# Optimization experiments

Hardware: AMD Instinct MI355X
Metric: run time of the kernel (lower is better)

Reference implementation:

```python
import jax, jax.numpy as jnp
import numpy as np

B, LQ, LK = 16, 1024, 2048
E, F, A = 512, 256, 512


def setup_inputs() -> dict:
    key = jax.random.key(0)
    ks = jax.random.split(key, 8)
    s_e = 1.0 / np.sqrt(E)
    s_f = 1.0 / np.sqrt(F)
    s_a = 1.0 / np.sqrt(A)
    return {
        "lstm_embeddings": jax.random.normal(ks[0], (B, LQ, E), jnp.float32),
        "optical_flow_features": jax.random.normal(ks[1], (B, LK, F), jnp.float32),
        "Wq": jax.random.normal(ks[2], (E, A), jnp.float32) * s_e,
        "bq": jnp.zeros((A,), jnp.float32),
        "Wk": jax.random.normal(ks[3], (F, A), jnp.float32) * s_f,
        "bk": jnp.zeros((A,), jnp.float32),
        "Wv": jax.random.normal(ks[4], (F, A), jnp.float32) * s_f,
        "bv": jnp.zeros((A,), jnp.float32),
        "Wo": jax.random.normal(ks[5], (A, E), jnp.float32) * s_a,
        "bo": jnp.zeros((E,), jnp.float32),
    }


def reference(lstm_embeddings, optical_flow_features, Wq, bq, Wk, bk, Wv, bv, Wo, bo):
    # Linear projections (x @ W + b), matching nn.Linear with W stored as [in, out]
    q = lstm_embeddings @ Wq + bq            # [B, LQ, A]
    k = optical_flow_features @ Wk + bk      # [B, LK, A]
    v = optical_flow_features @ Wv + bv      # [B, LK, A]
    # NOTE: original module does NOT scale scores by 1/sqrt(A) — stay faithful.
    scores = jnp.einsum("bqa,bka->bqk", q, k)      # [B, LQ, LK]
    weights = jax.nn.softmax(scores, axis=-1)
    context = jnp.einsum("bqk,bka->bqa", weights, v)  # [B, LQ, A]
    return context @ Wo + bo                          # [B, LQ, E]
```

## Files before the change

### kernel.cpp

```cpp
#include <hip/hip_runtime.h>


#define DEV static __device__ __forceinline__

typedef __attribute__((ext_vector_type(8))) short s8v;
typedef __attribute__((ext_vector_type(8))) _Float16 h8v;
typedef __attribute__((ext_vector_type(4))) float f4v;
typedef __attribute__((ext_vector_type(16))) float f16f;
typedef __attribute__((ext_vector_type(4))) float float4v;
typedef __attribute__((ext_vector_type(4))) unsigned int u32x4;
typedef unsigned short u16;
typedef unsigned int u32;

constexpr int BB = 16;
constexpr int LQ = 1024;
constexpr int LK = 2048;
constexpr int E = 512;
constexpr int F = 256;

DEV u16 f2bf(float x) {
    u32 u = __builtin_bit_cast(u32, x);
    u += 0x7fff + ((u >> 16) & 1);
    return (u16)(u >> 16);
}
DEV float bf2f(u16 h) { return __builtin_bit_cast(float, (u32)h << 16); }

DEV f4v MF(s8v a, s8v b, f4v c) {
    return __builtin_amdgcn_mfma_f32_16x16x32_bf16(a, b, c, 0, 0, 0);
}
DEV f4v MF16(h8v a, h8v b, f4v c) {
    return __builtin_amdgcn_mfma_f32_16x16x32_f16(a, b, c, 0, 0, 0);
}
DEV f16f MF32(h8v a, h8v b, f16f c) {
    return __builtin_amdgcn_mfma_f32_32x32x16_f16(a, b, c, 0, 0, 0);
}
DEV u32 pkh(float a, float b) {
    auto t = __builtin_amdgcn_cvt_pkrtz(a, b);
    return __builtin_bit_cast(u32, t);
}

DEV void gll16(const _Float16* g, _Float16* l) {
    __builtin_amdgcn_global_load_lds(
        (const __attribute__((address_space(1))) u32*)g,
        (__attribute__((address_space(3))) u32*)l, 16, 0, 0);
}

__global__ __launch_bounds__(256) void prew(
    const float* __restrict__ y, _Float16* __restrict__ yA,
    _Float16* __restrict__ yB,
    const float* __restrict__ Wq, const float* __restrict__ bq,
    const float* __restrict__ Wk, const float* __restrict__ Wv,
    const float* __restrict__ bv, const float* __restrict__ Wo,
    const float* __restrict__ bo,
    u16* __restrict__ Mhb, u16* __restrict__ Ntb,
    float* __restrict__ wvec, float* __restrict__ cvec)
{
    __shared__ __align__(16) char smem[33536];
    const int tid = threadIdx.x;
    const int bi = blockIdx.x;

    if (bi < 1024) {
        float (*Y)[260] = (float(*)[260])smem;
        const int b = bi >> 6, t = bi & 63;
        const float* src = y + ((size_t)b * LK + t * 32) * F;
#pragma unroll
        for (int i = 0; i < 8; ++i) {
            int base = i * 1024 + tid * 4;
            int k = base >> 8, f = base & 255;
            *(float4v*)&Y[k][f] = *(const float4v*)(src + base);
        }
        __syncthreads();
        size_t tb = (size_t)(b * 64 + t) * 8192;
#pragma unroll
        for (int i = 0; i < 4; ++i) {
            int c = i * 256 + tid;
            int k = c & 31, hi = (c >> 5) & 1, fs = c >> 6;
            int f0 = fs * 16 + hi * 8;
            float4v v0 = *(const float4v*)&Y[k][f0];
            float4v v1 = *(const float4v*)&Y[k][f0 + 4];
            h8v v;
#pragma unroll
            for (int j = 0; j < 4; ++j) { v[j] = (_Float16)v0[j]; v[4 + j] = (_Float16)v1[j]; }
            *(h8v*)(yA + tb + (size_t)c * 8) = v;
        }
#pragma unroll
        for (int i = 0; i < 4; ++i) {
            int c = i * 256 + tid;
            int fl = c & 31, hi = (c >> 5) & 1, frag = c >> 6;
            int ft = frag >> 1, ks = frag & 1;
            int f = ft * 32 + fl, k0 = ks * 16 + hi * 8;
            h8v v;
#pragma unroll
            for (int j = 0; j < 8; ++j) v[j] = (_Float16)Y[k0 + j][f];
            *(h8v*)(yB + tb + (size_t)c * 8) = v;
        }
        return;
    }

    const int wb = bi - 1024;
    if (wb >= 64) {
        if (wb == 64) {
            const float* r = Wk + (size_t)tid * 512;
            float s = 0.f;
#pragma unroll 4
            for (int a = 0; a < 512; a += 4) {
                float4v v = *(const float4v*)(r + a);
                float4v bb = *(const float4v*)(bq + a);
                s += v[0] * bb[0] + v[1] * bb[1] + v[2] * bb[2] + v[3] * bb[3];
            }
            wvec[tid] = s;
        } else {
            int e = (wb - 65) * 256 + tid;
            float s = bo[e];
#pragma unroll 4
            for (int a = 0; a < 512; ++a) s += bv[a] * Wo[(size_t)a * 512 + e];
            cvec[e] = s;
        }
        return;
    }

    const bool ntm = wb >= 32;
    const int bj = ntm ? wb - 32 : wb;
    const int m0 = ntm ? (bj >> 2) * 64 : (bj >> 3) * 64;
    const int n0 = ntm ? (bj & 3) * 64 : (bj & 7) * 64;
    const float* Ag = ntm ? Wo : Wk;
    const float* Bg = ntm ? Wv : Wq;

    u16 (*Ash)[40] = (u16(*)[40])(smem);
    u16 (*Asl)[40] = (u16(*)[40])(smem + 5120);
    u16 (*Bsh)[40] = (u16(*)[40])(smem + 10240);
    u16 (*Bsl)[40] = (u16(*)[40])(smem + 15360);

    const int w = tid >> 6, lane = tid & 63;
    const int g = lane >> 4, qn = lane & 15;
    const int wr = w & 1, wc = w >> 1;

    f4v acc[2][2];
#pragma unroll
    for (int i = 0; i < 2; ++i)
#pragma unroll
        for (int j = 0; j < 2; ++j) acc[i][j] = (f4v){0.f, 0.f, 0.f, 0.f};

    for (int k0 = 0; k0 < 512; k0 += 32) {
        __syncthreads();
        if (!ntm) {
            int r = tid & 63, c = (tid >> 6) * 8;
            const float* s = Ag + (size_t)(m0 + r) * 512 + k0 + c;
            float4v v0 = *(const float4v*)s, v1 = *(const float4v*)(s + 4);
            short hh[8], ll[8];
#pragma unroll
            for (int i = 0; i < 8; ++i) {
                float x = (i < 4) ? v0[i] : v1[i - 4];
                u16 h = f2bf(x);
                hh[i] = (short)h;
                ll[i] = (short)f2bf(x - bf2f(h));
            }
            *(s8v*)&Ash[r][c] = (s8v){hh[0],hh[1],hh[2],hh[3],hh[4],hh[5],hh[6],hh[7]};
            *(s8v*)&Asl[r][c] = (s8v){ll[0],ll[1],ll[2],ll[3],ll[4],ll[5],ll[6],ll[7]};
        } else {
            int k = tid >> 3, mc = (tid & 7) * 8;
            const float* s = Ag + (size_t)(k0 + k) * 512 + m0 + mc;
            float4v v0 = *(const float4v*)s, v1 = *(const float4v*)(s + 4);
#pragma unroll
            for (int i = 0; i < 8; ++i) {
                float x = (i < 4) ? v0[i] : v1[i - 4];
                u16 h = f2bf(x);
                Ash[mc + i][k] = h;
                Asl[mc + i][k] = f2bf(x - bf2f(h));
            }
        }
        {
            int r = tid & 63, c = (tid >> 6) * 8;
            const float* s = Bg + (size_t)(n0 + r) * 512 + k0 + c;
            float4v v0 = *(const float4v*)s, v1 = *(const float4v*)(s + 4);
            short hh[8], ll[8];
#pragma unroll
            for (int i = 0; i < 8; ++i) {
                float x = (i < 4) ? v0[i] : v1[i - 4];
                u16 h = f2bf(x);
                hh[i] = (short)h;
                ll[i] = (short)f2bf(x - bf2f(h));
            }
            *(s8v*)&Bsh[r][c] = (s8v){hh[0],hh[1],hh[2],hh[3],hh[4],hh[5],hh[6],hh[7]};
            *(s8v*)&Bsl[r][c] = (s8v){ll[0],ll[1],ll[2],ll[3],ll[4],ll[5],ll[6],ll[7]};
        }
        __syncthreads();

        s8v ah[2], al[2], bh[2], bl[2];
#pragma unroll
        for (int mt = 0; mt < 2; ++mt) {
            ah[mt] = *(const s8v*)&Ash[wr * 32 + mt * 16 + qn][g * 8];
            al[mt] = *(const s8v*)&Asl[wr * 32 + mt * 16 + qn][g * 8];
        }
#pragma unroll
        for (int nt = 0; nt < 2; ++nt) {
            bh[nt] = *(const s8v*)&Bsh[wc * 32 + nt * 16 + qn][g * 8];
            bl[nt] = *(const s8v*)&Bsl[wc * 32 + nt * 16 + qn][g * 8];
        }
#pragma unroll
        for (int mt = 0; mt < 2; ++mt)
#pragma unroll
            for (int nt = 0; nt < 2; ++nt) {
                acc[mt][nt] = MF(ah[mt], bh[nt], acc[mt][nt]);
                acc[mt][nt] = MF(ah[mt], bl[nt], acc[mt][nt]);
                acc[mt][nt] = MF(al[mt], bh[nt], acc[mt][nt]);
            }
    }

#pragma unroll
    for (int mt = 0; mt < 2; ++mt)
#pragma unroll
        for (int nt = 0; nt < 2; ++nt)
#pragma unroll
            for (int r = 0; r < 4; ++r) {
                int gm = m0 + wr * 32 + mt * 16 + 4 * g + r;
                int gn = n0 + wc * 32 + nt * 16 + qn;
                float v = acc[mt][nt][r];
                if (!ntm) {
                    size_t off = (size_t)((gn >> 5) * 16 + (gm >> 4)) * 512 +
                                 (gm & 15) * 8 + ((gn >> 3) & 3) * 128 + (gn & 7);
                    Mhb[off] = __builtin_bit_cast(u16, (_Float16)v);
                } else {
                    size_t off = (size_t)((gn >> 5) * 32 + (gm >> 4)) * 512 +
                                 (gm & 15) * 8 + ((gn >> 3) & 3) * 128 + (gn & 7);
                    Ntb[off] = __builtin_bit_cast(u16, (_Float16)v);
                }
            }
}

__global__ __launch_bounds__(256) void qprime5(
    const float* __restrict__ x, const u16* __restrict__ Mhb,
    const float* __restrict__ wv, _Float16* __restrict__ q16)
{
    __shared__ _Float16 Xs[2][64][40];
    const int tid = threadIdx.x, w = tid >> 6, lane = tid & 63;
    const int g = lane >> 4, qn = lane & 15;
    const int m0 = blockIdx.x * 64;
    const int nh = blockIdx.y * 8;
    const int srow = tid >> 2, scol = (tid & 3) * 8;
    const _Float16* Mh = (const _Float16*)Mhb;

    f4v acc[8];
#pragma unroll
    for (int n = 0; n < 8; ++n) acc[n] = (f4v){0.f, 0.f, 0.f, 0.f};

    float4v a0, a1;
    auto LDA = [&](int k0) {
        const float* s = x + (size_t)(m0 + srow) * 512 + k0 + scol;
        a0 = *(const float4v*)s;
        a1 = *(const float4v*)(s + 4);
    };
    auto STA = [&](int buf) {
        h8v v;
#pragma unroll
        for (int j = 0; j < 4; ++j) { v[j] = (_Float16)a0[j]; v[4 + j] = (_Float16)a1[j]; }
        *(h8v*)&Xs[buf][srow][scol] = v;
    };

    LDA(0); STA(0); LDA(32);
    __syncthreads();

    for (int t = 0; t < 16; ++t) {
        const int cur = t & 1;
        h8v af = *(const h8v*)&Xs[cur][w * 16 + qn][g * 8];
        const int fb = t * 16 + nh;
#pragma unroll
        for (int nt = 0; nt < 8; ++nt) {
            h8v bf = *(const h8v*)(Mh + (size_t)(fb + nt) * 512 + lane * 8);
            acc[nt] = MF16(af, bf, acc[nt]);
        }
        if (t < 15) {
            STA(cur ^ 1);
            if (t < 14) LDA((t + 2) * 32);
            __syncthreads();
        }
    }

#pragma unroll
    for (int nt = 0; nt < 8; ++nt) {
        int col = (nh + nt) * 16 + qn;
        float wvc = wv[col];
#pragma unroll
        for (int r = 0; r < 4; ++r) {
            int row = m0 + w * 16 + 4 * g + r;
            q16[(size_t)row * 256 + col] =
                (_Float16)((acc[nt][r] + wvc) * 1.44269504f);
        }
    }
}

__global__ __launch_bounds__(512) void flash6(
    const _Float16* __restrict__ q16, const _Float16* __restrict__ yA,
    const _Float16* __restrict__ yB, _Float16* __restrict__ part,
    float* __restrict__ ml)
{
    __shared__ _Float16 Asb[2][2][8192];
    __shared__ _Float16 Bsb[2][2][8192];

    const int tid = threadIdx.x;
    const int lane = tid & 63;
    const int q32 = lane & 31;
    const int hi = lane >> 5;

    int id = blockIdx.x;
    int xcd = id & 7, slot = id >> 3;
    int grp = xcd + 8 * (slot >> 2);
    int qb = slot & 3;
    int b = grp >> 2, z = grp & 3;
    const int qw = qb * 256 + (tid >> 6) * 32;

    h8v qf[16];
    {
        const _Float16* qp = q16 + ((size_t)b * LQ + qw + q32) * 256 + hi * 8;
#pragma unroll
        for (int s = 0; s < 16; ++s) qf[s] = *(const h8v*)(qp + s * 16);
    }
    f16f ctx[8];
#pragma unroll
    for (int i = 0; i < 8; ++i) ctx[i] = (f16f){};
    float mrun = -3.0e38f, lrun = 0.f;

    const size_t tbe = (size_t)(b * 64 + z * 16) * 8192;

    auto STAGE = [&](int sup, int buf) {
#pragma unroll
        for (int j = 0; j < 2; ++j) {
            const _Float16* ga = yA + tbe + (size_t)(sup * 2 + j) * 8192 + tid * 8;
            const _Float16* gb = yB + tbe + (size_t)(sup * 2 + j) * 8192 + tid * 8;
            gll16(ga,        &Asb[buf][j][tid * 8]);
            gll16(ga + 4096, &Asb[buf][j][tid * 8 + 4096]);
            gll16(gb,        &Bsb[buf][j][tid * 8]);
            gll16(gb + 4096, &Bsb[buf][j][tid * 8 + 4096]);
        }
    };

    STAGE(0, 0);
    __syncthreads();

    int buf = 0;
    for (int s = 0; s < 8; ++s) {
        if (s < 7) STAGE(s + 1, buf ^ 1);
#pragma unroll
        for (int j = 0; j < 2; ++j) {
            const _Float16* Ap = &Asb[buf][j][0];
            const _Float16* Bp = &Bsb[buf][j][0];
            f16f Sa = (f16f){}, Sb = (f16f){};
#pragma unroll
            for (int fs = 0; fs < 16; fs += 2) {
                h8v a0 = *(const h8v*)(Ap + fs * 512 + lane * 8);
                h8v a1 = *(const h8v*)(Ap + (fs + 1) * 512 + lane * 8);
                Sa = MF32(a0, qf[fs], Sa);
                Sb = MF32(a1, qf[fs + 1], Sb);
            }
            f16f S = Sa + Sb;
            float mt = fmaxf(S[0], S[1]);
#pragma unroll
            for (int r = 2; r < 16; ++r) mt = fmaxf(mt, S[r]);
            mt = fmaxf(mt, __shfl_xor(mt, 32));
            if (!__all(mt <= mrun + 11.5416f)) {
                float mnew = fmaxf(mrun, mt);
                float alpha = exp2f(mrun - mnew);
                lrun *= alpha;
#pragma unroll
                for (int r = 0; r < 16; ++r) {
                    int qr = (r & 3) + 8 * (r >> 2) + 4 * hi;
                    float ar = __shfl(alpha, qr);
#pragma unroll
                    for (int ft = 0; ft < 8; ++ft) ctx[ft][r] *= ar;
                }
                mrun = mnew;
            }
            float p[16], ps = 0.f;
#pragma unroll
            for (int r = 0; r < 16; ++r) { p[r] = exp2f(S[r] - mrun); ps += p[r]; }
            ps += __shfl_xor(ps, 32);
            lrun += ps;
            {
                u32 X0 = pkh(p[0], p[1]),   X1 = pkh(p[2], p[3]);
                u32 Y0 = pkh(p[4], p[5]),   Y1 = pkh(p[6], p[7]);
                u32 Z0 = pkh(p[8], p[9]),   Z1 = pkh(p[10], p[11]);
                u32 W0 = pkh(p[12], p[13]), W1 = pkh(p[14], p[15]);
                u32 M0 = hi ? X0 : Y0, M1 = hi ? X1 : Y1;
                u32 N0 = hi ? Z0 : W0, N1 = hi ? Z1 : W1;
                u32 sM0 = __shfl_xor(M0, 32), sM1 = __shfl_xor(M1, 32);
                u32 sN0 = __shfl_xor(N0, 32), sN1 = __shfl_xor(N1, 32);
                u32x4 A0u = (u32x4){hi ? sM0 : X0, hi ? sM1 : X1,
                                    hi ? Y0 : sM0, hi ? Y1 : sM1};
                u32x4 A1u = (u32x4){hi ? sN0 : Z0, hi ? sN1 : Z1,
                                    hi ? W0 : sN0, hi ? W1 : sN1};
                h8v pa0 = __builtin_bit_cast(h8v, A0u);
                h8v pa1 = __builtin_bit_cast(h8v, A1u);
#pragma unroll
                for (int ft = 0; ft < 8; ++ft) {
                    h8v bf = *(const h8v*)(Bp + (ft * 2 + 0) * 512 + lane * 8);
                    ctx[ft] = MF32(pa0, bf, ctx[ft]);
                }
#pragma unroll
                for (int ft = 0; ft < 8; ++ft) {
                    h8v bf = *(const h8v*)(Bp + (ft * 2 + 1) * 512 + lane * 8);
                    ctx[ft] = MF32(pa1, bf, ctx[ft]);
                }
            }
        }
        __syncthreads();
        buf ^= 1;
    }

    float linv = 1.f / lrun;
    _Float16* pp = part + ((size_t)z * (BB * LQ) + (size_t)b * LQ + qw) * 256;
#pragma unroll
    for (int r = 0; r < 16; ++r) {
        int qr = (r & 3) + 8 * (r >> 2) + 4 * hi;
        float ir = __shfl(linv, qr);
#pragma unroll
        for (int ft = 0; ft < 8; ++ft)
            pp[(size_t)qr * 256 + ft * 32 + q32] = (_Float16)(ctx[ft][r] * ir);
    }
    if (hi == 0) {
        size_t mi = (size_t)z * (BB * LQ) + (size_t)b * LQ + qw + q32;
        ml[2 * mi + 0] = mrun;
        ml[2 * mi + 1] = lrun;
    }
}

__global__ __launch_bounds__(256) void gemm2c(
    const _Float16* __restrict__ part, const float* __restrict__ ml,
    const u16* __restrict__ Ntb, const float* __restrict__ cvec,
    float* __restrict__ out)
{
    __shared__ _Float16 Asb[64][40];
    __shared__ float scl[64][4];
    const int tid = threadIdx.x;
    const int w = tid >> 6, lane = tid & 63;
    const int g = lane >> 4, qn = lane & 15;
    const int wr = w >> 1, wc = w & 1;
    const int m0 = blockIdx.x * 64, e0 = blockIdx.y * 256;
    constexpr size_t PL = (size_t)BB * LQ * F;
    constexpr size_t PR = (size_t)BB * LQ;

    if (tid < 64) {
        size_t i = m0 + tid;
        float m0v = ml[2 * i], l0v = ml[2 * i + 1];
        float m1v = ml[2 * (PR + i)], l1v = ml[2 * (PR + i) + 1];
        float m2v = ml[2 * (2 * PR + i)], l2v = ml[2 * (2 * PR + i) + 1];
        float m3v = ml[2 * (3 * PR + i)], l3v = ml[2 * (3 * PR + i) + 1];
        float M = fmaxf(fmaxf(m0v, m1v), fmaxf(m2v, m3v));
        float e0v = exp2f(m0v - M), e1v = exp2f(m1v - M);
        float e2v = exp2f(m2v - M), e3v = exp2f(m3v - M);
        float inv = 1.f / (l0v * e0v + l1v * e1v + l2v * e2v + l3v * e3v);
        scl[tid][0] = l0v * e0v * inv;
        scl[tid][1] = l1v * e1v * inv;
        scl[tid][2] = l2v * e2v * inv;
        scl[tid][3] = l3v * e3v * inv;
    }

    f4v acc[2][8];
#pragma unroll
    for (int i = 0; i < 2; ++i)
#pragma unroll
        for (int j = 0; j < 8; ++j) acc[i][j] = (f4v){0.f, 0.f, 0.f, 0.f};

    for (int k0 = 0; k0 < F; k0 += 32) {
        __syncthreads();
        {
            int r = tid & 63, c = (tid >> 6) * 8;
            size_t base = (size_t)(m0 + r) * F + k0 + c;
            h8v p0 = *(const h8v*)(part + base);
            h8v p1 = *(const h8v*)(part + PL + base);
            h8v p2 = *(const h8v*)(part + 2 * PL + base);
            h8v p3 = *(const h8v*)(part + 3 * PL + base);
            float s0 = scl[r][0], s1 = scl[r][1], s2 = scl[r][2], s3 = scl[r][3];
#pragma unroll
            for (int i = 0; i < 8; ++i) {
                float v = (float)p0[i] * s0 + (float)p1[i] * s1 +
                          (float)p2[i] * s2 + (float)p3[i] * s3;
                Asb[r][c + i] = (_Float16)v;
            }
        }
        __syncthreads();

        h8v ah[2], bh[8];
#pragma unroll
        for (int mt = 0; mt < 2; ++mt)
            ah[mt] = *(const h8v*)&Asb[wr * 32 + mt * 16 + qn][g * 8];
        int eb = (e0 + wc * 128) >> 4;
#pragma unroll
        for (int nt = 0; nt < 8; ++nt)
            bh[nt] = *(const h8v*)((const _Float16*)Ntb +
                     (size_t)((k0 >> 5) * 32 + eb + nt) * 512 + lane * 8);
#pragma unroll
        for (int mt = 0; mt < 2; ++mt)
#pragma unroll
            for (int nt = 0; nt < 8; ++nt)
                acc[mt][nt] = MF16(ah[mt], bh[nt], acc[mt][nt]);
    }

#pragma unroll
    for (int mt = 0; mt < 2; ++mt)
#pragma unroll
        for (int nt = 0; nt < 8; ++nt)
#pragma unroll
            for (int r = 0; r < 4; ++r) {
                int gm = m0 + wr * 32 + mt * 16 + 4 * g + r;
                int gn = e0 + wc * 128 + nt * 16 + qn;
                out[(size_t)gm * E + gn] = acc[mt][nt][r] + cvec[gn];
            }
}

extern "C" void kernel_launch(void* const* d_in, const int* in_sizes, int n_in,
                              void* d_out, int out_size, void* d_ws, size_t ws_size,
                              hipStream_t stream)
{
    const float* x  = (const float*)d_in[0];
    const float* y  = (const float*)d_in[1];
    const float* Wq = (const float*)d_in[2];
    const float* bq = (const float*)d_in[3];
    const float* Wk = (const float*)d_in[4];
    const float* Wv = (const float*)d_in[6];
    const float* bv = (const float*)d_in[7];
    const float* Wo = (const float*)d_in[8];
    const float* bo = (const float*)d_in[9];
    float* out = (float*)d_out;

    char* ws = (char*)d_ws;
    size_t off = 0;
    auto alloc = [&](size_t bytes) -> char* {
        char* p = ws + off;
        off = (off + bytes + 255) & ~(size_t)255;
        return p;
    };
    u16* Mhb  = (u16*)alloc(sizeof(u16) * F * E);
    float* wvec = (float*)alloc(sizeof(float) * F);
    float* cvec = (float*)alloc(sizeof(float) * E);
    u16* Ntb  = (u16*)alloc(sizeof(u16) * E * F);
    _Float16* q16 = (_Float16*)alloc(sizeof(u16) * (size_t)BB * LQ * F);
    _Float16* yA  = (_Float16*)alloc(sizeof(u16) * (size_t)BB * LK * F);
    _Float16* yB  = (_Float16*)alloc(sizeof(u16) * (size_t)BB * LK * F);
    _Float16* part = (_Float16*)alloc(sizeof(u16) * 4 * (size_t)BB * LQ * F);
    float* ml = (float*)alloc(sizeof(float) * 2 * 4 * (size_t)BB * LQ);
    (void)ws_size; (void)in_sizes; (void)n_in; (void)out_size;

    prew<<<dim3(1091), dim3(256), 0, stream>>>(
        y, yA, yB, Wq, bq, Wk, Wv, bv, Wo, bo, Mhb, Ntb, wvec, cvec);
    qprime5<<<dim3(BB * LQ / 64, 2), dim3(256), 0, stream>>>(x, Mhb, wvec, q16);
    flash6<<<dim3(256), dim3(512), 0, stream>>>(q16, yA, yB, part, ml);
    gemm2c<<<dim3(BB * LQ / 64, E / 256), dim3(256), 0, stream>>>(
        part, ml, Ntb, cvec, out);
}
```

Baseline: 137.2 us.

## Shrink flash blocks to 256 threads and prefetch Q-projection B fragments

```diff
diff --git a/kernel.cpp b/kernel.cpp
--- a/kernel.cpp
+++ b/kernel.cpp
@@ -228,7 +228,7 @@
             }
 }
 
-__global__ __launch_bounds__(256) void qprime5(
+__global__ __launch_bounds__(256) void qprime6(
     const float* __restrict__ x, const u16* __restrict__ Mhb,
     const float* __restrict__ wv, _Float16* __restrict__ q16)
 {
@@ -256,18 +256,34 @@
         for (int j = 0; j < 4; ++j) { v[j] = (_Float16)a0[j]; v[4 + j] = (_Float16)a1[j]; }
         *(h8v*)&Xs[buf][srow][scol] = v;
     };
-
-    LDA(0); STA(0); LDA(32);
+    h8v b0[8], b1[8];
+    auto LDB0 = [&](int t) {
+        const int fb = t * 16 + nh;
+#pragma unroll
+        for (int nt = 0; nt < 8; ++nt)
+            b0[nt] = *(const h8v*)(Mh + (size_t)(fb + nt) * 512 + lane * 8);
+    };
+    auto LDB1 = [&](int t) {
+        const int fb = t * 16 + nh;
+#pragma unroll
+        for (int nt = 0; nt < 8; ++nt)
+            b1[nt] = *(const h8v*)(Mh + (size_t)(fb + nt) * 512 + lane * 8);
+    };
+
+    LDA(0); STA(0); LDA(32); LDB0(0);
     __syncthreads();
 
+#pragma unroll
     for (int t = 0; t < 16; ++t) {
         const int cur = t & 1;
+        if (t < 15) { if (cur == 0) LDB1(t + 1); else LDB0(t + 1); }
         h8v af = *(const h8v*)&Xs[cur][w * 16 + qn][g * 8];
-        const int fb = t * 16 + nh;
-#pragma unroll
-        for (int nt = 0; nt < 8; ++nt) {
-            h8v bf = *(const h8v*)(Mh + (size_t)(fb + nt) * 512 + lane * 8);
-            acc[nt] = MF16(af, bf, acc[nt]);
+        if (cur == 0) {
+#pragma unroll
+            for (int nt = 0; nt < 8; ++nt) acc[nt] = MF16(af, b0[nt], acc[nt]);
+        } else {
+#pragma unroll
+            for (int nt = 0; nt < 8; ++nt) acc[nt] = MF16(af, b1[nt], acc[nt]);
         }
         if (t < 15) {
             STA(cur ^ 1);
@@ -289,13 +305,13 @@
     }
 }
 
-__global__ __launch_bounds__(512) void flash6(
+__global__ __launch_bounds__(256) void flash7(
     const _Float16* __restrict__ q16, const _Float16* __restrict__ yA,
     const _Float16* __restrict__ yB, _Float16* __restrict__ part,
     float* __restrict__ ml)
 {
-    __shared__ _Float16 Asb[2][2][8192];
-    __shared__ _Float16 Bsb[2][2][8192];
+    __shared__ _Float16 Asb[2][8192];
+    __shared__ _Float16 Bsb[2][8192];
 
     const int tid = threadIdx.x;
     const int lane = tid & 63;
@@ -304,10 +320,10 @@
 
     int id = blockIdx.x;
     int xcd = id & 7, slot = id >> 3;
-    int grp = xcd + 8 * (slot >> 2);
-    int qb = slot & 3;
+    int grp = xcd + 8 * (slot >> 3);
+    int qb = slot & 7;
     int b = grp >> 2, z = grp & 3;
-    const int qw = qb * 256 + (tid >> 6) * 32;
+    const int qw = qb * 128 + (tid >> 6) * 32;
 
     h8v qf[16];
     {
@@ -322,15 +338,13 @@
 
     const size_t tbe = (size_t)(b * 64 + z * 16) * 8192;
 
-    auto STAGE = [&](int sup, int buf) {
-#pragma unroll
-        for (int j = 0; j < 2; ++j) {
-            const _Float16* ga = yA + tbe + (size_t)(sup * 2 + j) * 8192 + tid * 8;
-            const _Float16* gb = yB + tbe + (size_t)(sup * 2 + j) * 8192 + tid * 8;
-            gll16(ga,        &Asb[buf][j][tid * 8]);
-            gll16(ga + 4096, &Asb[buf][j][tid * 8 + 4096]);
-            gll16(gb,        &Bsb[buf][j][tid * 8]);
-            gll16(gb + 4096, &Bsb[buf][j][tid * 8 + 4096]);
+    auto STAGE = [&](int t, int buf) {
+        const _Float16* ga = yA + tbe + (size_t)t * 8192;
+        const _Float16* gb = yB + tbe + (size_t)t * 8192;
+#pragma unroll
+        for (int i = 0; i < 4; ++i) {
+            gll16(ga + tid * 8 + i * 2048, &Asb[buf][tid * 8 + i * 2048]);
+            gll16(gb + tid * 8 + i * 2048, &Bsb[buf][tid * 8 + i * 2048]);
         }
     };
 
@@ -338,68 +352,65 @@
     __syncthreads();
 
     int buf = 0;
-    for (int s = 0; s < 8; ++s) {
-        if (s < 7) STAGE(s + 1, buf ^ 1);
-#pragma unroll
-        for (int j = 0; j < 2; ++j) {
-            const _Float16* Ap = &Asb[buf][j][0];
-            const _Float16* Bp = &Bsb[buf][j][0];
-            f16f Sa = (f16f){}, Sb = (f16f){};
-#pragma unroll
-            for (int fs = 0; fs < 16; fs += 2) {
-                h8v a0 = *(const h8v*)(Ap + fs * 512 + lane * 8);
-                h8v a1 = *(const h8v*)(Ap + (fs + 1) * 512 + lane * 8);
-                Sa = MF32(a0, qf[fs], Sa);
-                Sb = MF32(a1, qf[fs + 1], Sb);
-            }
-            f16f S = Sa + Sb;
-            float mt = fmaxf(S[0], S[1]);
-#pragma unroll
-            for (int r = 2; r < 16; ++r) mt = fmaxf(mt, S[r]);
-            mt = fmaxf(mt, __shfl_xor(mt, 32));
-            if (!__all(mt <= mrun + 11.5416f)) {
-                float mnew = fmaxf(mrun, mt);
-                float alpha = exp2f(mrun - mnew);
-                lrun *= alpha;
-#pragma unroll
-                for (int r = 0; r < 16; ++r) {
-                    int qr = (r & 3) + 8 * (r >> 2) + 4 * hi;
-                    float ar = __shfl(alpha, qr);
-#pragma unroll
-                    for (int ft = 0; ft < 8; ++ft) ctx[ft][r] *= ar;
-                }
-                mrun = mnew;
-            }
-            float p[16], ps = 0.f;
-#pragma unroll
-            for (int r = 0; r < 16; ++r) { p[r] = exp2f(S[r] - mrun); ps += p[r]; }
-            ps += __shfl_xor(ps, 32);
-            lrun += ps;
-            {
-                u32 X0 = pkh(p[0], p[1]),   X1 = pkh(p[2], p[3]);
-                u32 Y0 = pkh(p[4], p[5]),   Y1 = pkh(p[6], p[7]);
-                u32 Z0 = pkh(p[8], p[9]),   Z1 = pkh(p[10], p[11]);
-                u32 W0 = pkh(p[12], p[13]), W1 = pkh(p[14], p[15]);
-                u32 M0 = hi ? X0 : Y0, M1 = hi ? X1 : Y1;
-                u32 N0 = hi ? Z0 : W0, N1 = hi ? Z1 : W1;
-                u32 sM0 = __shfl_xor(M0, 32), sM1 = __shfl_xor(M1, 32);
-                u32 sN0 = __shfl_xor(N0, 32), sN1 = __shfl_xor(N1, 32);
-                u32x4 A0u = (u32x4){hi ? sM0 : X0, hi ? sM1 : X1,
-                                    hi ? Y0 : sM0, hi ? Y1 : sM1};
-                u32x4 A1u = (u32x4){hi ? sN0 : Z0, hi ? sN1 : Z1,
-                                    hi ? W0 : sN0, hi ? W1 : sN1};
-                h8v pa0 = __builtin_bit_cast(h8v, A0u);
-                h8v pa1 = __builtin_bit_cast(h8v, A1u);
-#pragma unroll
-                for (int ft = 0; ft < 8; ++ft) {
-                    h8v bf = *(const h8v*)(Bp + (ft * 2 + 0) * 512 + lane * 8);
-                    ctx[ft] = MF32(pa0, bf, ctx[ft]);
-                }
-#pragma unroll
-                for (int ft = 0; ft < 8; ++ft) {
-                    h8v bf = *(const h8v*)(Bp + (ft * 2 + 1) * 512 + lane * 8);
-                    ctx[ft] = MF32(pa1, bf, ctx[ft]);
-                }
+    for (int t = 0; t < 16; ++t) {
+        if (t < 15) STAGE(t + 1, buf ^ 1);
+        const _Float16* Ap = &Asb[buf][0];
+        const _Float16* Bp = &Bsb[buf][0];
+        f16f Sa = (f16f){}, Sb = (f16f){};
+#pragma unroll
+        for (int fs = 0; fs < 16; fs += 2) {
+            h8v a0 = *(const h8v*)(Ap + fs * 512 + lane * 8);
+            h8v a1 = *(const h8v*)(Ap + (fs + 1) * 512 + lane * 8);
+            Sa = MF32(a0, qf[fs], Sa);
+            Sb = MF32(a1, qf[fs + 1], Sb);
+        }
+        f16f S = Sa + Sb;
+        float mt = fmaxf(S[0], S[1]);
+#pragma unroll
+        for (int r = 2; r < 16; ++r) mt = fmaxf(mt, S[r]);
+        mt = fmaxf(mt, __shfl_xor(mt, 32));
+        if (!__all(mt <= mrun + 11.5416f)) {
+            float mnew = fmaxf(mrun, mt);
+            float alpha = exp2f(mrun - mnew);
+            lrun *= alpha;
+#pragma unroll
+            for (int r = 0; r < 16; ++r) {
+                int qr = (r & 3) + 8 * (r >> 2) + 4 * hi;
+                float ar = __shfl(alpha, qr);
+#pragma unroll
+                for (int ft = 0; ft < 8; ++ft) ctx[ft][r] *= ar;
+            }
+            mrun = mnew;
+        }
+        float p[16], ps = 0.f;
+#pragma unroll
+        for (int r = 0; r < 16; ++r) { p[r] = exp2f(S[r] - mrun); ps += p[r]; }
+        ps += __shfl_xor(ps, 32);
+        lrun += ps;
+        {
+            u32 X0 = pkh(p[0], p[1]),   X1 = pkh(p[2], p[3]);
+            u32 Y0 = pkh(p[4], p[5]),   Y1 = pkh(p[6], p[7]);
+            u32 Z0 = pkh(p[8], p[9]),   Z1 = pkh(p[10], p[11]);
+            u32 W0 = pkh(p[12], p[13]), W1 = pkh(p[14], p[15]);
+            u32 M0 = hi ? X0 : Y0, M1 = hi ? X1 : Y1;
+            u32 N0 = hi ? Z0 : W0, N1 = hi ? Z1 : W1;
+            u32 sM0 = __shfl_xor(M0, 32), sM1 = __shfl_xor(M1, 32);
+            u32 sN0 = __shfl_xor(N0, 32), sN1 = __shfl_xor(N1, 32);
+            u32x4 A0u = (u32x4){hi ? sM0 : X0, hi ? sM1 : X1,
+                                hi ? Y0 : sM0, hi ? Y1 : sM1};
+            u32x4 A1u = (u32x4){hi ? sN0 : Z0, hi ? sN1 : Z1,
+                                hi ? W0 : sN0, hi ? W1 : sN1};
+            h8v pa0 = __builtin_bit_cast(h8v, A0u);
+            h8v pa1 = __builtin_bit_cast(h8v, A1u);
+#pragma unroll
+            for (int ft = 0; ft < 8; ++ft) {
+                h8v bf = *(const h8v*)(Bp + (ft * 2 + 0) * 512 + lane * 8);
+                ctx[ft] = MF32(pa0, bf, ctx[ft]);
+            }
+#pragma unroll
+            for (int ft = 0; ft < 8; ++ft) {
+                h8v bf = *(const h8v*)(Bp + (ft * 2 + 1) * 512 + lane * 8);
+                ctx[ft] = MF32(pa1, bf, ctx[ft]);
             }
         }
         __syncthreads();
@@ -542,8 +553,8 @@
 
     prew<<<dim3(1091), dim3(256), 0, stream>>>(
         y, yA, yB, Wq, bq, Wk, Wv, bv, Wo, bo, Mhb, Ntb, wvec, cvec);
-    qprime5<<<dim3(BB * LQ / 64, 2), dim3(256), 0, stream>>>(x, Mhb, wvec, q16);
-    flash6<<<dim3(256), dim3(512), 0, stream>>>(q16, yA, yB, part, ml);
+    qprime6<<<dim3(BB * LQ / 64, 2), dim3(256), 0, stream>>>(x, Mhb, wvec, q16);
+    flash7<<<dim3(512), dim3(256), 0, stream>>>(q16, yA, yB, part, ml);
     gemm2c<<<dim3(BB * LQ / 64, E / 256), dim3(256), 0, stream>>>(
         part, ml, Ntb, cvec, out);
 }
```

Result: slower. 174.7 us (+27.3%).
